# Performance work log

Hardware: AMD Instinct MI355X
Metric: run time of the kernel (lower is better)

## Reference

```python
import jax, jax.numpy as jnp
import numpy as np

N_TRAJ = 4096
T = 128
LAT = 64          # latent_dim
NDATA = 64        # n_data_dim (values half of input)
INP = 2 * NDATA   # input_dim = values + mask
NGRU = 100        # gate hidden units
NODE = 100        # ode-func hidden units
TZ = 100          # transform_z0 hidden units


def setup_inputs() -> dict:
    key = jax.random.key(0)
    ks = jax.random.split(key, 16)
    vals = jax.random.normal(ks[0], (N_TRAJ, T, NDATA), jnp.float32)
    mask = (jax.random.uniform(ks[1], (N_TRAJ, T, NDATA)) > 0.5).astype(jnp.float32)
    data = jnp.concatenate([vals * mask, mask], axis=-1)  # [values | mask]
    tps = jnp.linspace(0.0, 2.0, T).astype(jnp.float32)   # uniform -> Euler branch every step
    D = 2 * LAT + INP
    def lin(k, i, o):
        return jax.random.normal(k, (i, o), jnp.float32) * 0.1
    return {
        "data": data, "tps": tps,
        "ug_w1": lin(ks[2], D, NGRU), "ug_b1": jnp.zeros(NGRU, jnp.float32),
        "ug_w2": lin(ks[3], NGRU, LAT), "ug_b2": jnp.zeros(LAT, jnp.float32),
        "rg_w1": lin(ks[4], D, NGRU), "rg_b1": jnp.zeros(NGRU, jnp.float32),
        "rg_w2": lin(ks[5], NGRU, LAT), "rg_b2": jnp.zeros(LAT, jnp.float32),
        "ns_w1": lin(ks[6], D, NGRU), "ns_b1": jnp.zeros(NGRU, jnp.float32),
        "ns_w2": lin(ks[7], NGRU, 2 * LAT), "ns_b2": jnp.zeros(2 * LAT, jnp.float32),
        "ode_w1": lin(ks[8], LAT, NODE), "ode_b1": jnp.zeros(NODE, jnp.float32),
        "ode_w2": lin(ks[9], NODE, LAT), "ode_b2": jnp.zeros(LAT, jnp.float32),
        "tz_w1": lin(ks[10], 2 * LAT, TZ), "tz_b1": jnp.zeros(TZ, jnp.float32),
        "tz_w2": lin(ks[11], TZ, 2 * LAT), "tz_b2": jnp.zeros(2 * LAT, jnp.float32),
    }


def reference(data, tps, ug_w1, ug_b1, ug_w2, ug_b2, rg_w1, rg_b1, rg_w2, rg_b2,
              ns_w1, ns_b1, ns_w2, ns_b2, ode_w1, ode_b1, ode_w2, ode_b2,
              tz_w1, tz_b1, tz_w2, tz_b2):
    n_traj = data.shape[0]

    def mlp2(x, w1, b1, w2, b2):
        return jnp.tanh(x @ w1 + b1) @ w2 + b2

    def gru(y_mu, y_std, x):
        yc = jnp.concatenate([y_mu, y_std, x], axis=-1)
        u = jax.nn.sigmoid(mlp2(yc, ug_w1, ug_b1, ug_w2, ug_b2))
        r = jax.nn.sigmoid(mlp2(yc, rg_w1, rg_b1, rg_w2, rg_b2))
        ns = mlp2(jnp.concatenate([y_mu * r, y_std * r, x], axis=-1),
                  ns_w1, ns_b1, ns_w2, ns_b2)
        new_state = ns[..., :LAT]
        new_std = jnp.abs(ns[..., LAT:])
        new_y = (1.0 - u) * new_state + u * y_mu
        new_y_std = (1.0 - u) * new_std + u * y_std
        m = x[..., NDATA:]  # mask half
        new_y = m * new_y + (1.0 - m) * y_mu
        new_y_std = m * new_y_std + (1.0 - m) * y_std
        return new_y, jnp.abs(new_y_std)

    # run_backwards=True: iterate i = T-1 .. 0
    xs = data[:, ::-1, :].transpose(1, 0, 2)       # (T, n_traj, INP)
    rev = tps[::-1]                                 # [t_{T-1}, ..., t_0]
    # first Euler dt = tps[-1] - (tps[-1] + 0.01) = -0.01; then dt_k = t_i - t_{i+1}
    dts = jnp.concatenate([jnp.full((1,), -0.01, jnp.float32), rev[1:] - rev[:-1]])

    def step(carry, inp):
        y, s = carry
        x, dt = inp
        y_ode = y + mlp2(y, ode_w1, ode_b1, ode_w2, ode_b2) * dt  # single Euler step
        y, s = gru(y_ode, s, x)
        return (y, s), None

    y0 = jnp.zeros((n_traj, LAT), data.dtype)
    (yi, yi_std), _ = jax.lax.scan(step, (y0, y0), (xs, dts))

    z = mlp2(jnp.concatenate([yi, yi_std], axis=-1), tz_w1, tz_b1, tz_w2, tz_b2)
    z0_mu = z[..., :LAT]
    z0_std = jnp.abs(z[..., LAT:])
    return z0_mu[None], z0_std[None]  # (1, n_traj, z0_dim) each
```

## Files before the change

kernel.cpp:

```cpp
#include <hip/hip_runtime.h>

typedef unsigned short u16;
typedef __attribute__((ext_vector_type(8))) short s8;
typedef __attribute__((ext_vector_type(4))) short s4;
typedef __attribute__((ext_vector_type(4))) float f4;

#define N_TRAJ 4096
#define TSTEPS 128
#define LATD   64
#define INPD   128

#define OB1 0
#define OB2 128
#define UB1 192
#define UB2 320
#define RB1 384
#define RB2 512
#define NB1 576
#define NB2 704
#define TB1 832
#define TB2 960
#define DTS 1088
#define NBIAS 1216

#define OFF_UG1 0
#define OFF_RG1 32768
#define OFF_NS1 65536
#define OFF_OD1 98304
#define OFF_UG2 106496
#define OFF_RG2 114688
#define OFF_NS2 122880
#define OFF_OD2 139264
#define OFF_TZ1 147456
#define OFF_TZ2 163840
#define PACK_ELEMS 180224

#define LUG2 0
#define LRG2 8192
#define LNS2 16384
#define LOD2 32768
#define LW2_ELEMS 40960

#define SYO 68

__device__ u16 g_pack[PACK_ELEMS];
__device__ float g_bias[NBIAS];

__device__ __forceinline__ float b2f(u16 u) {
    union { unsigned int i; float f; } v; v.i = ((unsigned int)u) << 16; return v.f;
}
__device__ __forceinline__ u16 f2b(float f) {
    unsigned int x = __float_as_uint(f);
    unsigned int r = (x + 0x7FFFu + ((x >> 16) & 1u)) >> 16;
    return (u16)r;
}
__device__ __forceinline__ unsigned int cvtpk(float lo, float hi) {
    unsigned int r;
    asm("v_cvt_pk_bf16_f32 %0, %1, %2" : "=v"(r) : "v"(lo), "v"(hi));
    return r;
}
__device__ __forceinline__ int is_f32(const void* tps) {
    return (*(const unsigned int*)tps) == 0u;
}
__device__ __forceinline__ float rdany(const void* a, int i, int isf32) {
    return isf32 ? ((const float*)a)[i] : b2f(((const u16*)a)[i]);
}
__device__ __forceinline__ float sigm(float x) {
    x = fminf(fmaxf(x, -30.f), 30.f);
    float e = __expf(-x);
    return __builtin_amdgcn_rcpf(1.f + e);
}
__device__ __forceinline__ float tanh_(float x) {
    x = fminf(fmaxf(x, -15.f), 15.f);
    float e = __expf(-2.f * x);
    return (1.f - e) * __builtin_amdgcn_rcpf(1.f + e);
}

__device__ __forceinline__ s8 aread(const u16* buf, int lane, int ks) {
    int row = lane & 15;
    int b = (ks << 6) + ((lane >> 4) << 4);
    int off = (row << 8) + (b ^ ((row & 7) << 4));
    return *(const s8*)((const char*)buf + off);
}
__device__ __forceinline__ void hwrite4(u16* buf, int traj, int ncol0, float a, float b, float c, float d) {
    int off = (traj << 8) + ((ncol0 << 1) ^ ((traj & 7) << 4));
    uint2 v;
    v.x = cvtpk(a, b);
    v.y = cvtpk(c, d);
    *(uint2*)((char*)buf + off) = v;
}
__device__ __forceinline__ s4 sread4(const u16* buf, int traj, int col0) {
    int off = (traj << 8) + ((col0 << 1) ^ ((traj & 7) << 4));
    return *(const s4*)((const char*)buf + off);
}
__device__ __forceinline__ s4 load_x4(const void* data, size_t elemIdx, int isf32) {
    s4 r;
    if (isf32) {
        f4 v = *(const f4*)((const float*)data + elemIdx);
#pragma unroll
        for (int j = 0; j < 4; ++j) r[j] = (short)f2b(v[j]);
    } else {
        r = *(const s4*)((const u16*)data + elemIdx);
    }
    return r;
}

struct PackP {
    const void* src[10];
    const void* tps;
    int Kr[10], Nr[10], KS[10], sz[10];
};

__global__ __launch_bounds__(256) void repack_kernel(PackP p) {
    int gid = blockIdx.x * 256 + threadIdx.x;
    if (gid >= PACK_ELEMS) return;
    int isf32 = is_f32(p.tps);
    int idx = gid, m = 0, base = 0;
    while (m < 10 && idx >= p.sz[m]) { idx -= p.sz[m]; base += p.sz[m]; ++m; }
    if (m >= 10) return;
    int i = idx & 7;
    int l = (idx >> 3) & 63;
    int rest = idx >> 9;
    int ks = rest % p.KS[m];
    int nt = rest / p.KS[m];
    int k = ks * 32 + ((l >> 4) << 3) + i;
    int n = nt * 16 + (l & 15);
    u16 v = 0;
    if (k < p.Kr[m] && n < p.Nr[m]) v = f2b(rdany(p.src[m], k * p.Nr[m] + n, isf32));
    g_pack[base + idx] = v;
}

struct PrepP {
    const void *tps, *ob1, *ob2, *ub1, *ub2, *rb1, *rb2, *nb1, *nb2, *tb1, *tb2;
};

__global__ __launch_bounds__(256) void prep_bias(PrepP p) {
    int isf32 = is_f32(p.tps);
    int tid = threadIdx.x;
    for (int i = tid; i < 128; i += 256) {
        g_bias[OB1 + i] = (i < 100) ? rdany(p.ob1, i, isf32) : 0.f;
        g_bias[UB1 + i] = (i < 100) ? rdany(p.ub1, i, isf32) : 0.f;
        g_bias[RB1 + i] = (i < 100) ? rdany(p.rb1, i, isf32) : 0.f;
        g_bias[NB1 + i] = (i < 100) ? rdany(p.nb1, i, isf32) : 0.f;
        g_bias[TB1 + i] = (i < 100) ? rdany(p.tb1, i, isf32) : 0.f;
        g_bias[NB2 + i] = rdany(p.nb2, i, isf32);
        g_bias[TB2 + i] = rdany(p.tb2, i, isf32);
        g_bias[DTS + i] = (i == 0) ? -0.01f
                                   : (rdany(p.tps, 127 - i, isf32) - rdany(p.tps, 128 - i, isf32));
    }
    for (int i = tid; i < 64; i += 256) {
        g_bias[OB2 + i] = rdany(p.ob2, i, isf32);
        g_bias[UB2 + i] = rdany(p.ub2, i, isf32);
        g_bias[RB2 + i] = rdany(p.rb2, i, isf32);
    }
}

struct MainP {
    const void *data, *tps;
    void* out;
};

#define WLOAD(off, KSn, nt, ks) (*(const s8*)(pk + (off) + (((((nt) * (KSn)) + (ks)) << 6) + lane) * 8))
#define LW(seg, nt, ks) (*(const s8*)(s_w2 + (seg) + ((((nt) * 4 + (ks)) << 6) + lane) * 8))
#define MFMA(wf, af, c) __builtin_amdgcn_mfma_f32_16x16x32_bf16((wf), (af), (c), 0, 0, 0)

__global__ __launch_bounds__(512, 2) void enc_main(MainP p) {
    __shared__ u16 s_x[2][2048];
    __shared__ u16 s_yc[2048];
    __shared__ u16 s_yc2[2048];
    __shared__ u16 s_hA[2048];
    __shared__ u16 s_hB[2048];
    __shared__ u16 s_w2[LW2_ELEMS];
    __shared__ float s_yo[16 * SYO];
    __shared__ float s_u[16 * SYO];
    __shared__ float s_b[NBIAS];

    int tid = threadIdx.x, lane = tid & 63, w = tid >> 6;
    int btraj = blockIdx.x << 4;
    const u16* pk = g_pack;
    int isf32 = is_f32(p.tps);

    for (int i = tid; i < NBIAS; i += 512) s_b[i] = g_bias[i];
    for (int i = tid; i < 2048; i += 512) s_yc[i] = 0;
    for (int i = tid; i < LW2_ELEMS / 8; i += 512)
        *(s8*)(s_w2 + i * 8) = *(const s8*)(pk + OFF_UG2 + i * 8);

    s8 wl1u[8], wl1r[8], wl1n[8];
    s8 wod1[2];
#pragma unroll
    for (int ks = 0; ks < 8; ++ks) {
        wl1u[ks] = WLOAD(OFF_UG1, 8, w, ks);
        wl1r[ks] = WLOAD(OFF_RG1, 8, w, ks);
        wl1n[ks] = WLOAD(OFF_NS1, 8, w, ks);
    }
    wod1[0] = WLOAD(OFF_OD1, 2, w, 0);
    wod1[1] = WLOAD(OFF_OD1, 2, w, 1);

    f4 ymu_r = {0.f, 0.f, 0.f, 0.f};
    f4 s_r = {0.f, 0.f, 0.f, 0.f};
    f4 yo_r = {0.f, 0.f, 0.f, 0.f};
    f4 u_r = {0.f, 0.f, 0.f, 0.f};

    int xrow = tid >> 5, xk = tid & 31;
    int xoff = (xrow << 8) + ((xk << 3) ^ ((xrow & 7) << 4));
    {
        s4 xr = load_x4(p.data, ((size_t)(btraj + xrow) * TSTEPS + 127) * INPD + (xk << 2), isf32);
        *(s4*)((char*)s_x[0] + xoff) = xr;
    }
    __syncthreads();

    const f4 zero4 = {0.f, 0.f, 0.f, 0.f};
    int traj = lane & 15;
    int nbase = (w << 4) + ((lane >> 4) << 2);

    for (int it = 0; it < TSTEPS; ++it) {
        int cur = it & 1;
        float dt = s_b[DTS + it];

        s4 xnext;
        if (it < 127) {
            xnext = load_x4(p.data, ((size_t)(btraj + xrow) * TSTEPS + (126 - it)) * INPD + (xk << 2), isf32);
        }

        f4 au = zero4, ar = zero4;

        {
            f4 ao = zero4;
            ao = MFMA(wod1[0], aread(s_yc, lane, 0), ao);
            ao = MFMA(wod1[1], aread(s_yc, lane, 1), ao);
#pragma unroll
            for (int ks = 2; ks < 4; ++ks) {
                s8 a = aread(s_yc, lane, ks);
                au = MFMA(wl1u[ks], a, au);
                ar = MFMA(wl1r[ks], a, ar);
            }
#pragma unroll
            for (int ks = 0; ks < 4; ++ks) {
                s8 a = aread(s_x[cur], lane, ks);
                au = MFMA(wl1u[4 + ks], a, au);
                ar = MFMA(wl1r[4 + ks], a, ar);
            }
            f4 b4 = *(const f4*)(s_b + OB1 + nbase);
            hwrite4(s_hA, traj, nbase, tanh_(ao[0] + b4[0]), tanh_(ao[1] + b4[1]),
                    tanh_(ao[2] + b4[2]), tanh_(ao[3] + b4[3]));
        }
        __syncthreads();

        if (w < 4) {
            s8 wod2[4];
#pragma unroll
            for (int ks = 0; ks < 4; ++ks) wod2[ks] = LW(LOD2, w, ks);
            f4 ac = zero4;
#pragma unroll
            for (int ks = 0; ks < 4; ++ks) ac = MFMA(wod2[ks], aread(s_hA, lane, ks), ac);
            f4 b4 = *(const f4*)(s_b + OB2 + nbase);
#pragma unroll
            for (int j = 0; j < 4; ++j) yo_r[j] = ymu_r[j] + (ac[j] + b4[j]) * dt;
            *(f4*)(s_yo + traj * SYO + nbase) = yo_r;
            hwrite4(s_yc, traj, nbase, yo_r[0], yo_r[1], yo_r[2], yo_r[3]);
        }
        __syncthreads();

        {
#pragma unroll
            for (int ks = 0; ks < 2; ++ks) {
                s8 a = aread(s_yc, lane, ks);
                au = MFMA(wl1u[ks], a, au);
                ar = MFMA(wl1r[ks], a, ar);
            }
            f4 bu4 = *(const f4*)(s_b + UB1 + nbase);
            f4 br4 = *(const f4*)(s_b + RB1 + nbase);
            hwrite4(s_hA, traj, nbase, tanh_(au[0] + bu4[0]), tanh_(au[1] + bu4[1]),
                    tanh_(au[2] + bu4[2]), tanh_(au[3] + bu4[3]));
            hwrite4(s_hB, traj, nbase, tanh_(ar[0] + br4[0]), tanh_(ar[1] + br4[1]),
                    tanh_(ar[2] + br4[2]), tanh_(ar[3] + br4[3]));
        }
        __syncthreads();

        f4 an = zero4;
        {
#pragma unroll
            for (int ks = 0; ks < 4; ++ks)
                an = MFMA(wl1n[4 + ks], aread(s_x[cur], lane, ks), an);
        }
        if (w < 4) {
            s8 w2[4];
#pragma unroll
            for (int ks = 0; ks < 4; ++ks) w2[ks] = LW(LUG2, w, ks);
            f4 uac = zero4;
#pragma unroll
            for (int ks = 0; ks < 4; ++ks) uac = MFMA(w2[ks], aread(s_hA, lane, ks), uac);
            f4 b4 = *(const f4*)(s_b + UB2 + nbase);
#pragma unroll
            for (int j = 0; j < 4; ++j) u_r[j] = sigm(uac[j] + b4[j]);
            *(f4*)(s_u + traj * SYO + nbase) = u_r;
        } else {
            s8 w2[4];
#pragma unroll
            for (int ks = 0; ks < 4; ++ks) w2[ks] = LW(LRG2, w - 4, ks);
            f4 rac = zero4;
#pragma unroll
            for (int ks = 0; ks < 4; ++ks) rac = MFMA(w2[ks], aread(s_hB, lane, ks), rac);
            int sb = nbase - 64;
            f4 b4 = *(const f4*)(s_b + RB2 + sb);
            f4 yo4 = *(const f4*)(s_yo + traj * SYO + sb);
            f4 rv;
#pragma unroll
            for (int j = 0; j < 4; ++j) rv[j] = sigm(rac[j] + b4[j]);
            hwrite4(s_yc2, traj, sb, yo4[0] * rv[0], yo4[1] * rv[1], yo4[2] * rv[2], yo4[3] * rv[3]);
            hwrite4(s_yc2, traj, nbase, s_r[0] * rv[0], s_r[1] * rv[1], s_r[2] * rv[2], s_r[3] * rv[3]);
        }
        __syncthreads();

        {
#pragma unroll
            for (int ks = 0; ks < 4; ++ks) an = MFMA(wl1n[ks], aread(s_yc2, lane, ks), an);
            f4 b4 = *(const f4*)(s_b + NB1 + nbase);
            hwrite4(s_hA, traj, nbase, tanh_(an[0] + b4[0]), tanh_(an[1] + b4[1]),
                    tanh_(an[2] + b4[2]), tanh_(an[3] + b4[3]));
        }
        __syncthreads();

        {
            s8 wn2[4];
#pragma unroll
            for (int ks = 0; ks < 4; ++ks) wn2[ks] = LW(LNS2, w, ks);
            f4 fn = zero4;
#pragma unroll
            for (int ks = 0; ks < 4; ++ks) fn = MFMA(wn2[ks], aread(s_hA, lane, ks), fn);
            if (it < 127) *(s4*)((char*)s_x[cur ^ 1] + xoff) = xnext;

            f4 b4 = *(const f4*)(s_b + NB2 + nbase);
            if (w < 4) {
                s4 mm = sread4(s_x[cur], traj, 64 + nbase);
#pragma unroll
                for (int j = 0; j < 4; ++j) {
                    float nsv = fn[j] + b4[j];
                    float m = b2f((u16)mm[j]);
                    float mg = m * (1.f - u_r[j]);
                    ymu_r[j] = yo_r[j] + mg * (nsv - yo_r[j]);
                }
                hwrite4(s_yc, traj, nbase, ymu_r[0], ymu_r[1], ymu_r[2], ymu_r[3]);
            } else {
                int sb = nbase - 64;
                s4 mm = sread4(s_x[cur], traj, nbase);
                f4 u4 = *(const f4*)(s_u + traj * SYO + sb);
#pragma unroll
                for (int j = 0; j < 4; ++j) {
                    float nsv = fabsf(fn[j] + b4[j]);
                    float m = b2f((u16)mm[j]);
                    float mg = m * (1.f - u4[j]);
                    float nss = s_r[j] + mg * (nsv - s_r[j]);
                    s_r[j] = fabsf(nss);
                }
                hwrite4(s_yc, traj, nbase, s_r[0], s_r[1], s_r[2], s_r[3]);
            }
        }
        __syncthreads();
    }

    s8 wt1[4], wt2[4];
#pragma unroll
    for (int ks = 0; ks < 4; ++ks) {
        wt1[ks] = WLOAD(OFF_TZ1, 4, w, ks);
        wt2[ks] = WLOAD(OFF_TZ2, 4, w, ks);
    }
    {
        f4 t1 = zero4;
#pragma unroll
        for (int ks = 0; ks < 4; ++ks) t1 = MFMA(wt1[ks], aread(s_yc, lane, ks), t1);
        f4 b4 = *(const f4*)(s_b + TB1 + nbase);
        hwrite4(s_hA, traj, nbase, tanh_(t1[0] + b4[0]), tanh_(t1[1] + b4[1]),
                tanh_(t1[2] + b4[2]), tanh_(t1[3] + b4[3]));
    }
    __syncthreads();
    {
        f4 t2 = zero4;
#pragma unroll
        for (int ks = 0; ks < 4; ++ks) t2 = MFMA(wt2[ks], aread(s_hA, lane, ks), t2);
        f4 b4 = *(const f4*)(s_b + TB2 + nbase);
        int gtraj = btraj + traj;
        f4 z;
        size_t base;
        if (w < 4) {
#pragma unroll
            for (int j = 0; j < 4; ++j) z[j] = t2[j] + b4[j];
            base = (size_t)gtraj * 64 + nbase;
        } else {
#pragma unroll
            for (int j = 0; j < 4; ++j) z[j] = fabsf(t2[j] + b4[j]);
            base = (size_t)N_TRAJ * 64 + (size_t)gtraj * 64 + (nbase - 64);
        }
        if (isf32) {
            *(f4*)((float*)p.out + base) = z;
        } else {
            uint2 pv;
            pv.x = cvtpk(z[0], z[1]);
            pv.y = cvtpk(z[2], z[3]);
            *(uint2*)((u16*)p.out + base) = pv;
        }
    }
}

extern "C" void kernel_launch(void* const* d_in, const int* in_sizes, int n_in,
                              void* d_out, int out_size, void* d_ws, size_t ws_size,
                              hipStream_t stream) {
    PackP pp;
    const int srcIdx[10] = {2, 6, 10, 14, 4, 8, 12, 16, 18, 20};
    const int Kr[10] = {256, 256, 256, 64, 100, 100, 100, 100, 128, 100};
    const int Nr[10] = {100, 100, 100, 100, 64, 64, 128, 64, 100, 128};
    const int KS[10] = {8, 8, 8, 2, 4, 4, 4, 4, 4, 4};
    const int NT[10] = {8, 8, 8, 8, 4, 4, 8, 4, 8, 8};
    for (int i = 0; i < 10; ++i) {
        pp.src[i] = d_in[srcIdx[i]];
        pp.Kr[i] = Kr[i];
        pp.Nr[i] = Nr[i];
        pp.KS[i] = KS[i];
        pp.sz[i] = KS[i] * NT[i] * 512;
    }
    pp.tps = d_in[1];
    repack_kernel<<<(PACK_ELEMS + 255) / 256, 256, 0, stream>>>(pp);

    PrepP bp;
    bp.tps = d_in[1];
    bp.ob1 = d_in[15]; bp.ob2 = d_in[17];
    bp.ub1 = d_in[3];  bp.ub2 = d_in[5];
    bp.rb1 = d_in[7];  bp.rb2 = d_in[9];
    bp.nb1 = d_in[11]; bp.nb2 = d_in[13];
    bp.tb1 = d_in[19]; bp.tb2 = d_in[21];
    prep_bias<<<1, 256, 0, stream>>>(bp);

    MainP mp;
    mp.data = d_in[0];
    mp.tps = d_in[1];
    mp.out = d_out;
    enc_main<<<N_TRAJ / 16, 512, 0, stream>>>(mp);
}
```

Measured before the change: 380.4 us.

## Fold ODE output layer into gate first layers to remove a barrier stage

```diff
diff --git a/kernel.cpp b/kernel.cpp
--- a/kernel.cpp
+++ b/kernel.cpp
@@ -21,7 +21,9 @@
 #define TB1 832
 #define TB2 960
 #define DTS 1088
-#define NBIAS 1216
+#define BXU 1216
+#define BXR 1344
+#define NBIAS 1472
 
 #define OFF_UG1 0
 #define OFF_RG1 32768
@@ -42,8 +44,11 @@
 #define LW2_ELEMS 40960
 
 #define SYO 68
+#define MUPACK 16384
 
 __device__ u16 g_pack[PACK_ELEMS];
+__device__ u16 g_mupack[MUPACK];
+__device__ u16 g_mrpack[MUPACK];
 __device__ float g_bias[NBIAS];
 
 __device__ __forceinline__ float b2f(u16 u) {
@@ -130,8 +135,34 @@
     g_pack[base + idx] = v;
 }
 
+struct MuP {
+    const void *uw1, *rw1, *ow2, *tps;
+};
+
+__global__ __launch_bounds__(256) void muprep_kernel(MuP p) {
+    int gid = blockIdx.x * 256 + threadIdx.x;
+    if (gid >= 2 * MUPACK) return;
+    int isf32 = is_f32(p.tps);
+    int m = gid >> 14;
+    int idx = gid & (MUPACK - 1);
+    int i = idx & 7;
+    int l = (idx >> 3) & 63;
+    int rest = idx >> 9;
+    int ks = rest & 3;
+    int nt = rest >> 2;
+    int k = ks * 32 + ((l >> 4) << 3) + i;
+    int n = nt * 16 + (l & 15);
+    const void* w1 = m ? p.rw1 : p.uw1;
+    float acc = 0.f;
+    if (k < 100 && n < 100) {
+        for (int c = 0; c < 64; ++c)
+            acc += rdany(p.ow2, k * 64 + c, isf32) * rdany(w1, c * 100 + n, isf32);
+    }
+    (m ? g_mrpack : g_mupack)[idx] = f2b(acc);
+}
+
 struct PrepP {
-    const void *tps, *ob1, *ob2, *ub1, *ub2, *rb1, *rb2, *nb1, *nb2, *tb1, *tb2;
+    const void *tps, *ob1, *ob2, *ub1, *ub2, *rb1, *rb2, *nb1, *nb2, *tb1, *tb2, *uw1, *rw1;
 };
 
 __global__ __launch_bounds__(256) void prep_bias(PrepP p) {
@@ -147,6 +178,16 @@
         g_bias[TB2 + i] = rdany(p.tb2, i, isf32);
         g_bias[DTS + i] = (i == 0) ? -0.01f
                                    : (rdany(p.tps, 127 - i, isf32) - rdany(p.tps, 128 - i, isf32));
+        float bu = 0.f, br = 0.f;
+        if (i < 100) {
+            for (int c = 0; c < 64; ++c) {
+                float o = rdany(p.ob2, c, isf32);
+                bu += o * rdany(p.uw1, c * 100 + i, isf32);
+                br += o * rdany(p.rw1, c * 100 + i, isf32);
+            }
+        }
+        g_bias[BXU + i] = bu;
+        g_bias[BXR + i] = br;
     }
     for (int i = tid; i < 64; i += 256) {
         g_bias[OB2 + i] = rdany(p.ob2, i, isf32);
@@ -162,6 +203,7 @@
 
 #define WLOAD(off, KSn, nt, ks) (*(const s8*)(pk + (off) + (((((nt) * (KSn)) + (ks)) << 6) + lane) * 8))
 #define LW(seg, nt, ks) (*(const s8*)(s_w2 + (seg) + ((((nt) * 4 + (ks)) << 6) + lane) * 8))
+#define MULOAD(arr, ks) (*(const s8*)((arr) + (((w * 4 + (ks)) << 6) + lane) * 8))
 #define MFMA(wf, af, c) __builtin_amdgcn_mfma_f32_16x16x32_bf16((wf), (af), (c), 0, 0, 0)
 
 __global__ __launch_bounds__(512, 2) void enc_main(MainP p) {
@@ -170,6 +212,7 @@
     __shared__ u16 s_yc2[2048];
     __shared__ u16 s_hA[2048];
     __shared__ u16 s_hB[2048];
+    __shared__ u16 s_hC[2048];
     __shared__ u16 s_w2[LW2_ELEMS];
     __shared__ float s_yo[16 * SYO];
     __shared__ float s_u[16 * SYO];
@@ -187,6 +230,7 @@
 
     s8 wl1u[8], wl1r[8], wl1n[8];
     s8 wod1[2];
+    s8 wMu[4], wMr[4];
 #pragma unroll
     for (int ks = 0; ks < 8; ++ks) {
         wl1u[ks] = WLOAD(OFF_UG1, 8, w, ks);
@@ -195,6 +239,11 @@
     }
     wod1[0] = WLOAD(OFF_OD1, 2, w, 0);
     wod1[1] = WLOAD(OFF_OD1, 2, w, 1);
+#pragma unroll
+    for (int ks = 0; ks < 4; ++ks) {
+        wMu[ks] = MULOAD(g_mupack, ks);
+        wMr[ks] = MULOAD(g_mrpack, ks);
+    }
 
     f4 ymu_r = {0.f, 0.f, 0.f, 0.f};
     f4 s_r = {0.f, 0.f, 0.f, 0.f};
@@ -222,12 +271,19 @@
             xnext = load_x4(p.data, ((size_t)(btraj + xrow) * TSTEPS + (126 - it)) * INPD + (xk << 2), isf32);
         }
 
-        f4 au = zero4, ar = zero4;
+        f4 au = zero4, ar = zero4, an = zero4;
+        s8 ax[4];
 
         {
+            s8 a0 = aread(s_yc, lane, 0);
+            s8 a1 = aread(s_yc, lane, 1);
             f4 ao = zero4;
-            ao = MFMA(wod1[0], aread(s_yc, lane, 0), ao);
-            ao = MFMA(wod1[1], aread(s_yc, lane, 1), ao);
+            ao = MFMA(wod1[0], a0, ao);
+            ao = MFMA(wod1[1], a1, ao);
+            au = MFMA(wl1u[0], a0, au);
+            au = MFMA(wl1u[1], a1, au);
+            ar = MFMA(wl1r[0], a0, ar);
+            ar = MFMA(wl1r[1], a1, ar);
 #pragma unroll
             for (int ks = 2; ks < 4; ++ks) {
                 s8 a = aread(s_yc, lane, ks);
@@ -236,9 +292,9 @@
             }
 #pragma unroll
             for (int ks = 0; ks < 4; ++ks) {
-                s8 a = aread(s_x[cur], lane, ks);
-                au = MFMA(wl1u[4 + ks], a, au);
-                ar = MFMA(wl1r[4 + ks], a, ar);
+                ax[ks] = aread(s_x[cur], lane, ks);
+                au = MFMA(wl1u[4 + ks], ax[ks], au);
+                ar = MFMA(wl1r[4 + ks], ax[ks], ar);
             }
             f4 b4 = *(const f4*)(s_b + OB1 + nbase);
             hwrite4(s_hA, traj, nbase, tanh_(ao[0] + b4[0]), tanh_(ao[1] + b4[1]),
@@ -246,69 +302,74 @@
         }
         __syncthreads();
 
-        if (w < 4) {
-            s8 wod2[4];
-#pragma unroll
-            for (int ks = 0; ks < 4; ++ks) wod2[ks] = LW(LOD2, w, ks);
-            f4 ac = zero4;
-#pragma unroll
-            for (int ks = 0; ks < 4; ++ks) ac = MFMA(wod2[ks], aread(s_hA, lane, ks), ac);
-            f4 b4 = *(const f4*)(s_b + OB2 + nbase);
-#pragma unroll
-            for (int j = 0; j < 4; ++j) yo_r[j] = ymu_r[j] + (ac[j] + b4[j]) * dt;
-            *(f4*)(s_yo + traj * SYO + nbase) = yo_r;
-            hwrite4(s_yc, traj, nbase, yo_r[0], yo_r[1], yo_r[2], yo_r[3]);
-        }
-        __syncthreads();
-
         {
-#pragma unroll
-            for (int ks = 0; ks < 2; ++ks) {
-                s8 a = aread(s_yc, lane, ks);
-                au = MFMA(wl1u[ks], a, au);
-                ar = MFMA(wl1r[ks], a, ar);
-            }
+            f4 mu = zero4, mr = zero4, oc = zero4;
+#pragma unroll
+            for (int ks = 0; ks < 4; ++ks) {
+                s8 h = aread(s_hA, lane, ks);
+                mu = MFMA(wMu[ks], h, mu);
+                mr = MFMA(wMr[ks], h, mr);
+                if (w < 4) {
+                    s8 wod2 = LW(LOD2, w, ks);
+                    oc = MFMA(wod2, h, oc);
+                }
+            }
+#pragma unroll
+            for (int ks = 0; ks < 4; ++ks)
+                an = MFMA(wl1n[4 + ks], ax[ks], an);
+
             f4 bu4 = *(const f4*)(s_b + UB1 + nbase);
             f4 br4 = *(const f4*)(s_b + RB1 + nbase);
-            hwrite4(s_hA, traj, nbase, tanh_(au[0] + bu4[0]), tanh_(au[1] + bu4[1]),
-                    tanh_(au[2] + bu4[2]), tanh_(au[3] + bu4[3]));
-            hwrite4(s_hB, traj, nbase, tanh_(ar[0] + br4[0]), tanh_(ar[1] + br4[1]),
-                    tanh_(ar[2] + br4[2]), tanh_(ar[3] + br4[3]));
+            f4 xu4 = *(const f4*)(s_b + BXU + nbase);
+            f4 xr4 = *(const f4*)(s_b + BXR + nbase);
+            hwrite4(s_hB, traj, nbase,
+                    tanh_(au[0] + dt * (mu[0] + xu4[0]) + bu4[0]),
+                    tanh_(au[1] + dt * (mu[1] + xu4[1]) + bu4[1]),
+                    tanh_(au[2] + dt * (mu[2] + xu4[2]) + bu4[2]),
+                    tanh_(au[3] + dt * (mu[3] + xu4[3]) + bu4[3]));
+            hwrite4(s_hC, traj, nbase,
+                    tanh_(ar[0] + dt * (mr[0] + xr4[0]) + br4[0]),
+                    tanh_(ar[1] + dt * (mr[1] + xr4[1]) + br4[1]),
+                    tanh_(ar[2] + dt * (mr[2] + xr4[2]) + br4[2]),
+                    tanh_(ar[3] + dt * (mr[3] + xr4[3]) + br4[3]));
+            if (w < 4) {
+                f4 b4 = *(const f4*)(s_b + OB2 + nbase);
+#pragma unroll
+                for (int j = 0; j < 4; ++j) yo_r[j] = ymu_r[j] + (oc[j] + b4[j]) * dt;
+                *(f4*)(s_yo + traj * SYO + nbase) = yo_r;
+            }
         }
         __syncthreads();
 
-        f4 an = zero4;
         {
-#pragma unroll
-            for (int ks = 0; ks < 4; ++ks)
-                an = MFMA(wl1n[4 + ks], aread(s_x[cur], lane, ks), an);
-        }
-        if (w < 4) {
-            s8 w2[4];
-#pragma unroll
-            for (int ks = 0; ks < 4; ++ks) w2[ks] = LW(LUG2, w, ks);
-            f4 uac = zero4;
-#pragma unroll
-            for (int ks = 0; ks < 4; ++ks) uac = MFMA(w2[ks], aread(s_hA, lane, ks), uac);
-            f4 b4 = *(const f4*)(s_b + UB2 + nbase);
-#pragma unroll
-            for (int j = 0; j < 4; ++j) u_r[j] = sigm(uac[j] + b4[j]);
-            *(f4*)(s_u + traj * SYO + nbase) = u_r;
-        } else {
-            s8 w2[4];
-#pragma unroll
-            for (int ks = 0; ks < 4; ++ks) w2[ks] = LW(LRG2, w - 4, ks);
-            f4 rac = zero4;
-#pragma unroll
-            for (int ks = 0; ks < 4; ++ks) rac = MFMA(w2[ks], aread(s_hB, lane, ks), rac);
-            int sb = nbase - 64;
-            f4 b4 = *(const f4*)(s_b + RB2 + sb);
-            f4 yo4 = *(const f4*)(s_yo + traj * SYO + sb);
-            f4 rv;
-#pragma unroll
-            for (int j = 0; j < 4; ++j) rv[j] = sigm(rac[j] + b4[j]);
-            hwrite4(s_yc2, traj, sb, yo4[0] * rv[0], yo4[1] * rv[1], yo4[2] * rv[2], yo4[3] * rv[3]);
-            hwrite4(s_yc2, traj, nbase, s_r[0] * rv[0], s_r[1] * rv[1], s_r[2] * rv[2], s_r[3] * rv[3]);
+            if (it < 127) *(s4*)((char*)s_x[cur ^ 1] + xoff) = xnext;
+            if (w < 4) {
+                f4 uac = zero4;
+#pragma unroll
+                for (int ks = 0; ks < 4; ++ks) {
+                    s8 w2 = LW(LUG2, w, ks);
+                    uac = MFMA(w2, aread(s_hB, lane, ks), uac);
+                }
+                f4 b4 = *(const f4*)(s_b + UB2 + nbase);
+#pragma unroll
+                for (int j = 0; j < 4; ++j) u_r[j] = sigm(uac[j] + b4[j]);
+                *(f4*)(s_u + traj * SYO + nbase) = u_r;
+            } else {
+                f4 rac = zero4;
+#pragma unroll
+                for (int ks = 0; ks < 4; ++ks) {
+                    s8 w2 = LW(LRG2, w - 4, ks);
+                    rac = MFMA(w2, aread(s_hC, lane, ks), rac);
+                }
+                int sb = nbase - 64;
+                f4 b4 = *(const f4*)(s_b + RB2 + sb);
+                f4 yo4 = *(const f4*)(s_yo + traj * SYO + sb);
+                f4 rv;
+#pragma unroll
+                for (int j = 0; j < 4; ++j) rv[j] = sigm(rac[j] + b4[j]);
+                hwrite4(s_yc2, traj, sb, yo4[0] * rv[0], yo4[1] * rv[1], yo4[2] * rv[2], yo4[3] * rv[3]);
+                hwrite4(s_yc2, traj, nbase, s_r[0] * rv[0], s_r[1] * rv[1], s_r[2] * rv[2], s_r[3] * rv[3]);
+            }
         }
         __syncthreads();
 
@@ -322,14 +383,12 @@
         __syncthreads();
 
         {
-            s8 wn2[4];
-#pragma unroll
-            for (int ks = 0; ks < 4; ++ks) wn2[ks] = LW(LNS2, w, ks);
             f4 fn = zero4;
 #pragma unroll
-            for (int ks = 0; ks < 4; ++ks) fn = MFMA(wn2[ks], aread(s_hA, lane, ks), fn);
-            if (it < 127) *(s4*)((char*)s_x[cur ^ 1] + xoff) = xnext;
-
+            for (int ks = 0; ks < 4; ++ks) {
+                s8 wn2 = LW(LNS2, w, ks);
+                fn = MFMA(wn2, aread(s_hA, lane, ks), fn);
+            }
             f4 b4 = *(const f4*)(s_b + NB2 + nbase);
             if (w < 4) {
                 s4 mm = sread4(s_x[cur], traj, 64 + nbase);
@@ -421,6 +480,13 @@
     pp.tps = d_in[1];
     repack_kernel<<<(PACK_ELEMS + 255) / 256, 256, 0, stream>>>(pp);
 
+    MuP mup;
+    mup.uw1 = d_in[2];
+    mup.rw1 = d_in[6];
+    mup.ow2 = d_in[16];
+    mup.tps = d_in[1];
+    muprep_kernel<<<(2 * MUPACK + 255) / 256, 256, 0, stream>>>(mup);
+
     PrepP bp;
     bp.tps = d_in[1];
     bp.ob1 = d_in[15]; bp.ob2 = d_in[17];
@@ -428,6 +494,7 @@
     bp.rb1 = d_in[7];  bp.rb2 = d_in[9];
     bp.nb1 = d_in[11]; bp.nb2 = d_in[13];
     bp.tb1 = d_in[19]; bp.tb2 = d_in[21];
+    bp.uw1 = d_in[2];  bp.rw1 = d_in[6];
     prep_bias<<<1, 256, 0, stream>>>(bp);
 
     MainP mp;
```

Result: slower. 402.9 us (+5.9%).

## Keep second-layer weights in registers and split MFMA accumulator chains

Applied to the files above, without the earlier changes.

```diff
diff --git a/kernel.cpp b/kernel.cpp
--- a/kernel.cpp
+++ b/kernel.cpp
@@ -34,12 +34,6 @@
 #define OFF_TZ1 147456
 #define OFF_TZ2 163840
 #define PACK_ELEMS 180224
-
-#define LUG2 0
-#define LRG2 8192
-#define LNS2 16384
-#define LOD2 32768
-#define LW2_ELEMS 40960
 
 #define SYO 68
 
@@ -161,7 +155,6 @@
 };
 
 #define WLOAD(off, KSn, nt, ks) (*(const s8*)(pk + (off) + (((((nt) * (KSn)) + (ks)) << 6) + lane) * 8))
-#define LW(seg, nt, ks) (*(const s8*)(s_w2 + (seg) + ((((nt) * 4 + (ks)) << 6) + lane) * 8))
 #define MFMA(wf, af, c) __builtin_amdgcn_mfma_f32_16x16x32_bf16((wf), (af), (c), 0, 0, 0)
 
 __global__ __launch_bounds__(512, 2) void enc_main(MainP p) {
@@ -170,7 +163,6 @@
     __shared__ u16 s_yc2[2048];
     __shared__ u16 s_hA[2048];
     __shared__ u16 s_hB[2048];
-    __shared__ u16 s_w2[LW2_ELEMS];
     __shared__ float s_yo[16 * SYO];
     __shared__ float s_u[16 * SYO];
     __shared__ float s_b[NBIAS];
@@ -182,11 +174,10 @@
 
     for (int i = tid; i < NBIAS; i += 512) s_b[i] = g_bias[i];
     for (int i = tid; i < 2048; i += 512) s_yc[i] = 0;
-    for (int i = tid; i < LW2_ELEMS / 8; i += 512)
-        *(s8*)(s_w2 + i * 8) = *(const s8*)(pk + OFF_UG2 + i * 8);
 
     s8 wl1u[8], wl1r[8], wl1n[8];
     s8 wod1[2];
+    s8 wod2[4], w2x[4], wn2[4];
 #pragma unroll
     for (int ks = 0; ks < 8; ++ks) {
         wl1u[ks] = WLOAD(OFF_UG1, 8, w, ks);
@@ -195,6 +186,18 @@
     }
     wod1[0] = WLOAD(OFF_OD1, 2, w, 0);
     wod1[1] = WLOAD(OFF_OD1, 2, w, 1);
+#pragma unroll
+    for (int ks = 0; ks < 4; ++ks) {
+        wod2[ks] = WLOAD(OFF_OD2, 4, (w & 3), ks);
+        wn2[ks] = WLOAD(OFF_NS2, 4, w, ks);
+    }
+    if (w < 4) {
+#pragma unroll
+        for (int ks = 0; ks < 4; ++ks) w2x[ks] = WLOAD(OFF_UG2, 4, w, ks);
+    } else {
+#pragma unroll
+        for (int ks = 0; ks < 4; ++ks) w2x[ks] = WLOAD(OFF_RG2, 4, w - 4, ks);
+    }
 
     f4 ymu_r = {0.f, 0.f, 0.f, 0.f};
     f4 s_r = {0.f, 0.f, 0.f, 0.f};
@@ -222,24 +225,34 @@
             xnext = load_x4(p.data, ((size_t)(btraj + xrow) * TSTEPS + (126 - it)) * INPD + (xk << 2), isf32);
         }
 
-        f4 au = zero4, ar = zero4;
+        f4 au0 = zero4, au1 = zero4, ar0 = zero4, ar1 = zero4;
+        f4 an0 = zero4, an1 = zero4;
+        s8 ax0, ax1, ax2, ax3;
 
         {
+            ax0 = aread(s_x[cur], lane, 0);
+            ax1 = aread(s_x[cur], lane, 1);
+            ax2 = aread(s_x[cur], lane, 2);
+            ax3 = aread(s_x[cur], lane, 3);
+            s8 ay0 = aread(s_yc, lane, 0);
+            s8 ay1 = aread(s_yc, lane, 1);
+            s8 ay2 = aread(s_yc, lane, 2);
+            s8 ay3 = aread(s_yc, lane, 3);
             f4 ao = zero4;
-            ao = MFMA(wod1[0], aread(s_yc, lane, 0), ao);
-            ao = MFMA(wod1[1], aread(s_yc, lane, 1), ao);
-#pragma unroll
-            for (int ks = 2; ks < 4; ++ks) {
-                s8 a = aread(s_yc, lane, ks);
-                au = MFMA(wl1u[ks], a, au);
-                ar = MFMA(wl1r[ks], a, ar);
-            }
-#pragma unroll
-            for (int ks = 0; ks < 4; ++ks) {
-                s8 a = aread(s_x[cur], lane, ks);
-                au = MFMA(wl1u[4 + ks], a, au);
-                ar = MFMA(wl1r[4 + ks], a, ar);
-            }
+            ao = MFMA(wod1[0], ay0, ao);
+            ao = MFMA(wod1[1], ay1, ao);
+            au0 = MFMA(wl1u[2], ay2, au0);
+            ar0 = MFMA(wl1r[2], ay2, ar0);
+            au0 = MFMA(wl1u[3], ay3, au0);
+            ar0 = MFMA(wl1r[3], ay3, ar0);
+            au0 = MFMA(wl1u[4], ax0, au0);
+            ar0 = MFMA(wl1r[4], ax0, ar0);
+            au0 = MFMA(wl1u[5], ax1, au0);
+            ar0 = MFMA(wl1r[5], ax1, ar0);
+            au1 = MFMA(wl1u[6], ax2, au1);
+            ar1 = MFMA(wl1r[6], ax2, ar1);
+            au1 = MFMA(wl1u[7], ax3, au1);
+            ar1 = MFMA(wl1r[7], ax3, ar1);
             f4 b4 = *(const f4*)(s_b + OB1 + nbase);
             hwrite4(s_hA, traj, nbase, tanh_(ao[0] + b4[0]), tanh_(ao[1] + b4[1]),
                     tanh_(ao[2] + b4[2]), tanh_(ao[3] + b4[3]));
@@ -247,87 +260,91 @@
         __syncthreads();
 
         if (w < 4) {
-            s8 wod2[4];
-#pragma unroll
-            for (int ks = 0; ks < 4; ++ks) wod2[ks] = LW(LOD2, w, ks);
-            f4 ac = zero4;
-#pragma unroll
-            for (int ks = 0; ks < 4; ++ks) ac = MFMA(wod2[ks], aread(s_hA, lane, ks), ac);
+            f4 ac0 = zero4, ac1 = zero4;
+            ac0 = MFMA(wod2[0], aread(s_hA, lane, 0), ac0);
+            ac1 = MFMA(wod2[2], aread(s_hA, lane, 2), ac1);
+            ac0 = MFMA(wod2[1], aread(s_hA, lane, 1), ac0);
+            ac1 = MFMA(wod2[3], aread(s_hA, lane, 3), ac1);
             f4 b4 = *(const f4*)(s_b + OB2 + nbase);
 #pragma unroll
-            for (int j = 0; j < 4; ++j) yo_r[j] = ymu_r[j] + (ac[j] + b4[j]) * dt;
+            for (int j = 0; j < 4; ++j) yo_r[j] = ymu_r[j] + (ac0[j] + ac1[j] + b4[j]) * dt;
             *(f4*)(s_yo + traj * SYO + nbase) = yo_r;
             hwrite4(s_yc, traj, nbase, yo_r[0], yo_r[1], yo_r[2], yo_r[3]);
+        } else {
+            an0 = MFMA(wl1n[4], ax0, an0);
+            an1 = MFMA(wl1n[6], ax2, an1);
+            an0 = MFMA(wl1n[5], ax1, an0);
+            an1 = MFMA(wl1n[7], ax3, an1);
         }
         __syncthreads();
 
         {
-#pragma unroll
-            for (int ks = 0; ks < 2; ++ks) {
-                s8 a = aread(s_yc, lane, ks);
-                au = MFMA(wl1u[ks], a, au);
-                ar = MFMA(wl1r[ks], a, ar);
-            }
+            s8 a0 = aread(s_yc, lane, 0);
+            s8 a1 = aread(s_yc, lane, 1);
+            au1 = MFMA(wl1u[0], a0, au1);
+            ar1 = MFMA(wl1r[0], a0, ar1);
+            au1 = MFMA(wl1u[1], a1, au1);
+            ar1 = MFMA(wl1r[1], a1, ar1);
             f4 bu4 = *(const f4*)(s_b + UB1 + nbase);
             f4 br4 = *(const f4*)(s_b + RB1 + nbase);
-            hwrite4(s_hA, traj, nbase, tanh_(au[0] + bu4[0]), tanh_(au[1] + bu4[1]),
-                    tanh_(au[2] + bu4[2]), tanh_(au[3] + bu4[3]));
-            hwrite4(s_hB, traj, nbase, tanh_(ar[0] + br4[0]), tanh_(ar[1] + br4[1]),
-                    tanh_(ar[2] + br4[2]), tanh_(ar[3] + br4[3]));
-        }
-        __syncthreads();
-
-        f4 an = zero4;
-        {
-#pragma unroll
-            for (int ks = 0; ks < 4; ++ks)
-                an = MFMA(wl1n[4 + ks], aread(s_x[cur], lane, ks), an);
-        }
+            hwrite4(s_hA, traj, nbase,
+                    tanh_(au0[0] + au1[0] + bu4[0]), tanh_(au0[1] + au1[1] + bu4[1]),
+                    tanh_(au0[2] + au1[2] + bu4[2]), tanh_(au0[3] + au1[3] + bu4[3]));
+            hwrite4(s_hB, traj, nbase,
+                    tanh_(ar0[0] + ar1[0] + br4[0]), tanh_(ar0[1] + ar1[1] + br4[1]),
+                    tanh_(ar0[2] + ar1[2] + br4[2]), tanh_(ar0[3] + ar1[3] + br4[3]));
+        }
+        __syncthreads();
+
         if (w < 4) {
-            s8 w2[4];
-#pragma unroll
-            for (int ks = 0; ks < 4; ++ks) w2[ks] = LW(LUG2, w, ks);
-            f4 uac = zero4;
-#pragma unroll
-            for (int ks = 0; ks < 4; ++ks) uac = MFMA(w2[ks], aread(s_hA, lane, ks), uac);
+            an0 = MFMA(wl1n[4], ax0, an0);
+            an1 = MFMA(wl1n[6], ax2, an1);
+            an0 = MFMA(wl1n[5], ax1, an0);
+            an1 = MFMA(wl1n[7], ax3, an1);
+            f4 uac0 = zero4, uac1 = zero4;
+            uac0 = MFMA(w2x[0], aread(s_hA, lane, 0), uac0);
+            uac1 = MFMA(w2x[2], aread(s_hA, lane, 2), uac1);
+            uac0 = MFMA(w2x[1], aread(s_hA, lane, 1), uac0);
+            uac1 = MFMA(w2x[3], aread(s_hA, lane, 3), uac1);
             f4 b4 = *(const f4*)(s_b + UB2 + nbase);
 #pragma unroll
-            for (int j = 0; j < 4; ++j) u_r[j] = sigm(uac[j] + b4[j]);
+            for (int j = 0; j < 4; ++j) u_r[j] = sigm(uac0[j] + uac1[j] + b4[j]);
             *(f4*)(s_u + traj * SYO + nbase) = u_r;
         } else {
-            s8 w2[4];
-#pragma unroll
-            for (int ks = 0; ks < 4; ++ks) w2[ks] = LW(LRG2, w - 4, ks);
-            f4 rac = zero4;
-#pragma unroll
-            for (int ks = 0; ks < 4; ++ks) rac = MFMA(w2[ks], aread(s_hB, lane, ks), rac);
+            f4 rac0 = zero4, rac1 = zero4;
+            rac0 = MFMA(w2x[0], aread(s_hB, lane, 0), rac0);
+            rac1 = MFMA(w2x[2], aread(s_hB, lane, 2), rac1);
+            rac0 = MFMA(w2x[1], aread(s_hB, lane, 1), rac0);
+            rac1 = MFMA(w2x[3], aread(s_hB, lane, 3), rac1);
             int sb = nbase - 64;
             f4 b4 = *(const f4*)(s_b + RB2 + sb);
             f4 yo4 = *(const f4*)(s_yo + traj * SYO + sb);
             f4 rv;
 #pragma unroll
-            for (int j = 0; j < 4; ++j) rv[j] = sigm(rac[j] + b4[j]);
+            for (int j = 0; j < 4; ++j) rv[j] = sigm(rac0[j] + rac1[j] + b4[j]);
             hwrite4(s_yc2, traj, sb, yo4[0] * rv[0], yo4[1] * rv[1], yo4[2] * rv[2], yo4[3] * rv[3]);
             hwrite4(s_yc2, traj, nbase, s_r[0] * rv[0], s_r[1] * rv[1], s_r[2] * rv[2], s_r[3] * rv[3]);
         }
         __syncthreads();
 
         {
-#pragma unroll
-            for (int ks = 0; ks < 4; ++ks) an = MFMA(wl1n[ks], aread(s_yc2, lane, ks), an);
+            an0 = MFMA(wl1n[0], aread(s_yc2, lane, 0), an0);
+            an1 = MFMA(wl1n[2], aread(s_yc2, lane, 2), an1);
+            an0 = MFMA(wl1n[1], aread(s_yc2, lane, 1), an0);
+            an1 = MFMA(wl1n[3], aread(s_yc2, lane, 3), an1);
             f4 b4 = *(const f4*)(s_b + NB1 + nbase);
-            hwrite4(s_hA, traj, nbase, tanh_(an[0] + b4[0]), tanh_(an[1] + b4[1]),
-                    tanh_(an[2] + b4[2]), tanh_(an[3] + b4[3]));
+            hwrite4(s_hA, traj, nbase,
+                    tanh_(an0[0] + an1[0] + b4[0]), tanh_(an0[1] + an1[1] + b4[1]),
+                    tanh_(an0[2] + an1[2] + b4[2]), tanh_(an0[3] + an1[3] + b4[3]));
         }
         __syncthreads();
 
         {
-            s8 wn2[4];
-#pragma unroll
-            for (int ks = 0; ks < 4; ++ks) wn2[ks] = LW(LNS2, w, ks);
-            f4 fn = zero4;
-#pragma unroll
-            for (int ks = 0; ks < 4; ++ks) fn = MFMA(wn2[ks], aread(s_hA, lane, ks), fn);
+            f4 fn0 = zero4, fn1 = zero4;
+            fn0 = MFMA(wn2[0], aread(s_hA, lane, 0), fn0);
+            fn1 = MFMA(wn2[2], aread(s_hA, lane, 2), fn1);
+            fn0 = MFMA(wn2[1], aread(s_hA, lane, 1), fn0);
+            fn1 = MFMA(wn2[3], aread(s_hA, lane, 3), fn1);
             if (it < 127) *(s4*)((char*)s_x[cur ^ 1] + xoff) = xnext;
 
             f4 b4 = *(const f4*)(s_b + NB2 + nbase);
@@ -335,7 +352,7 @@
                 s4 mm = sread4(s_x[cur], traj, 64 + nbase);
 #pragma unroll
                 for (int j = 0; j < 4; ++j) {
-                    float nsv = fn[j] + b4[j];
+                    float nsv = fn0[j] + fn1[j] + b4[j];
                     float m = b2f((u16)mm[j]);
                     float mg = m * (1.f - u_r[j]);
                     ymu_r[j] = yo_r[j] + mg * (nsv - yo_r[j]);
@@ -347,7 +364,7 @@
                 f4 u4 = *(const f4*)(s_u + traj * SYO + sb);
 #pragma unroll
                 for (int j = 0; j < 4; ++j) {
-                    float nsv = fabsf(fn[j] + b4[j]);
+                    float nsv = fabsf(fn0[j] + fn1[j] + b4[j]);
                     float m = b2f((u16)mm[j]);
                     float mg = m * (1.f - u4[j]);
                     float nss = s_r[j] + mg * (nsv - s_r[j]);
```

Result: faster. 358.2 us (-5.8%).
